# Kernel optimization log

Measured on AMD Instinct MI355X. Metric: run time of the kernel, lower is better.

## Reference

```python
import jax, jax.numpy as jnp
import numpy as np
import math

B, S, D_MODEL = 4, 2048, 1024
H, D_QK, D_V = 16, 64, 64


def setup_inputs() -> dict:
    key = jax.random.key(0)
    ks = jax.random.split(key, 12)
    s = 0.02
    return {
        "input_q": jax.random.normal(ks[0], (B, S, D_MODEL), jnp.float32),
        "input_k": jax.random.normal(ks[1], (B, S, D_MODEL), jnp.float32),
        "input_v": jax.random.normal(ks[2], (B, S, D_MODEL), jnp.float32),
        # per-head projection weights stacked over heads: [H, out, d_model] (torch Linear layout)
        "WQw": jax.random.normal(ks[3], (H, D_QK, D_MODEL), jnp.float32) * s,
        "WQb": jax.random.normal(ks[4], (H, D_QK), jnp.float32) * s,
        "WKw": jax.random.normal(ks[5], (H, D_QK, D_MODEL), jnp.float32) * s,
        "WKb": jax.random.normal(ks[6], (H, D_QK), jnp.float32) * s,
        "WVw": jax.random.normal(ks[7], (H, D_V, D_MODEL), jnp.float32) * s,
        "WVb": jax.random.normal(ks[8], (H, D_V), jnp.float32) * s,
        # output projection: Linear(H*D_V, D_MODEL)
        "Ww": jax.random.normal(ks[9], (D_MODEL, H * D_V), jnp.float32) * s,
        "Wb": jax.random.normal(ks[10], (D_MODEL,), jnp.float32) * s,
    }


def _mha(input_q, input_k, input_v, WQw, WQb, WKw, WKb, WVw, WVb, Ww, Wb):
    # per-head projections: [B,H,S,d]
    Q = jnp.einsum("bsd,hed->bhse", input_q, WQw) + WQb[None, :, None, :]
    K = jnp.einsum("bsd,hed->bhse", input_k, WKw) + WKb[None, :, None, :]
    V = jnp.einsum("bsd,hvd->bhsv", input_v, WVw) + WVb[None, :, None, :]
    scores = jnp.einsum("bhse,bhte->bhst", Q, K)  # [B,H,S,S]
    # causal mask added BEFORE division by sqrt(d_model), as in original
    causal = jnp.triu(jnp.full((S, S), -jnp.inf, scores.dtype), k=1)
    scores = (scores + causal) / math.sqrt(D_MODEL)  # NOTE: d_model, not d_qk
    attn = jax.nn.softmax(scores, axis=-1)
    ctx = jnp.einsum("bhst,bhtv->bhsv", attn, V)  # [B,H,S,D_V]
    concat = ctx.transpose(0, 2, 1, 3).reshape(B, S, H * D_V)  # head-order concat
    return concat @ Ww.T + Wb


def reference(input_q, input_k, input_v, WQw, WQb, WKw, WKb, WVw, WVb, Ww, Wb):
    return _mha(input_q, input_k, input_v, WQw, WQb, WKw, WKb, WVw, WVb, Ww, Wb)
```

## Files before the change

kernel.cpp:

```cpp
#include <hip/hip_runtime.h>
#include <hip/hip_bf16.h>

typedef __attribute__((ext_vector_type(8))) short bf16x8;
typedef __attribute__((ext_vector_type(4))) short bf16x4;
typedef __attribute__((ext_vector_type(4))) float f32x4;
typedef __attribute__((ext_vector_type(16))) float f32x16;

#define MFMA16(a, b, c) __builtin_amdgcn_mfma_f32_16x16x32_bf16(a, b, c, 0, 0, 0)
#define MFMA32(a, b, c) __builtin_amdgcn_mfma_f32_32x32x16_bf16(a, b, c, 0, 0, 0)

__device__ __forceinline__ unsigned short f2bfn(float f) {
#if defined(__gfx950__)
  __bf16 h = (__bf16)f;
  return __builtin_bit_cast(unsigned short, h);
#else
  union { float f; unsigned u; } x; x.f = f;
  unsigned r = x.u + 0x7fffu + ((x.u >> 16) & 1u);
  return (unsigned short)(r >> 16);
#endif
}

__device__ __forceinline__ void plswap(unsigned& a, unsigned& b) {
  auto r = __builtin_amdgcn_permlane32_swap(a, b, false, false);
  a = r[0];
  b = r[1];
}

__device__ __forceinline__ unsigned cvtpk(float lo, float hi) {
  unsigned w;
  asm("v_cvt_pk_bf16_f32 %0, %1, %2" : "=v"(w) : "v"(lo), "v"(hi));
  return w;
}

__device__ __forceinline__ void cvt_body(const float* __restrict__ s,
                                         unsigned short* __restrict__ d, int n8) {
  int i = blockIdx.x * blockDim.x + threadIdx.x;
  int st = gridDim.x * blockDim.x;
  for (; i < n8; i += st) {
    const float4* sp = reinterpret_cast<const float4*>(s) + 2 * (size_t)i;
    float4 a = sp[0], b = sp[1];
    bf16x8 o;
    o[0] = (short)f2bfn(a.x); o[1] = (short)f2bfn(a.y);
    o[2] = (short)f2bfn(a.z); o[3] = (short)f2bfn(a.w);
    o[4] = (short)f2bfn(b.x); o[5] = (short)f2bfn(b.y);
    o[6] = (short)f2bfn(b.z); o[7] = (short)f2bfn(b.w);
    reinterpret_cast<bf16x8*>(d)[i] = o;
  }
}

__global__ void cvt1_kernel(const float* __restrict__ s, unsigned short* __restrict__ d, int n8) {
  cvt_body(s, d, n8);
}

__global__ void cvt_w_kernel(const float* s0, const float* s1, const float* s2, const float* s3,
                             unsigned short* d0, unsigned short* d1, unsigned short* d2,
                             unsigned short* d3, int n8) {
  const float* s; unsigned short* d;
  switch (blockIdx.y) {
    case 0: s = s0; d = d0; break;
    case 1: s = s1; d = d1; break;
    case 2: s = s2; d = d2; break;
    default: s = s3; d = d3; break;
  }
  cvt_body(s, d, n8);
}

template <int MODE>
__global__ __launch_bounds__(256) void gemm_kernel(
    const unsigned short* __restrict__ Av, const unsigned short* __restrict__ Bv,
    const float* __restrict__ bias, void* __restrict__ outv,
    int M, int N, int K) {
  constexpr int BM = 128, BN = 128, BK = 64;
  __shared__ __align__(16) unsigned short As[2][BM * BK];
  __shared__ __align__(16) unsigned short Bs[2][BN * BK];
  const int tid = threadIdx.x;
  const int lane = tid & 63, wave = tid >> 6;
  const int wr = wave >> 1, wc = wave & 1;
  const int m0 = blockIdx.y * BM, n0 = blockIdx.x * BN;
  const int rb = lane & 15, g = lane >> 4;
  const int swz = ((lane & 7) ^ ((lane >> 3) & 7)) * 8;
  f32x4 acc[4][4] = {};

  const unsigned short* Ab = Av + (size_t)m0 * K;
  const unsigned short* Bb = Bv + (size_t)n0 * K;

  auto stage = [&](int buf, int k0) {
#pragma unroll
    for (int i = 0; i < 4; ++i) {
      const int c = wave * 256 + i * 64 + lane;
      const int r = c >> 3;
      __builtin_amdgcn_global_load_lds(
          (const __attribute__((address_space(1))) unsigned int*)(Ab + (size_t)r * K + k0 + swz),
          (__attribute__((address_space(3))) unsigned int*)&As[buf][c * 8], 16, 0, 0);
      __builtin_amdgcn_global_load_lds(
          (const __attribute__((address_space(1))) unsigned int*)(Bb + (size_t)r * K + k0 + swz),
          (__attribute__((address_space(3))) unsigned int*)&Bs[buf][c * 8], 16, 0, 0);
    }
  };

  const int nt = K / BK;
  stage(0, 0);
  int cur = 0;
  for (int t = 0; t < nt; ++t) {
    __syncthreads();
    if (t + 1 < nt) stage(cur ^ 1, (t + 1) * BK);
    const unsigned short* A_ = As[cur];
    const unsigned short* B_ = Bs[cur];
#pragma unroll
    for (int kc = 0; kc < 2; ++kc) {
      bf16x8 af[4], bfr[4];
#pragma unroll
      for (int mi = 0; mi < 4; ++mi)
        af[mi] = *reinterpret_cast<const bf16x8*>(
            &A_[(wr * 64 + mi * 16 + rb) * 64 + (((kc * 4 + g) ^ (rb & 7)) * 8)]);
#pragma unroll
      for (int ni = 0; ni < 4; ++ni)
        bfr[ni] = *reinterpret_cast<const bf16x8*>(
            &B_[(wc * 64 + ni * 16 + rb) * 64 + (((kc * 4 + g) ^ (rb & 7)) * 8)]);
#pragma unroll
      for (int mi = 0; mi < 4; ++mi)
#pragma unroll
        for (int ni = 0; ni < 4; ++ni)
          acc[mi][ni] = MFMA16(af[mi], bfr[ni], acc[mi][ni]);
    }
    cur ^= 1;
  }

#pragma unroll
  for (int mi = 0; mi < 4; ++mi) {
#pragma unroll
    for (int ni = 0; ni < 4; ++ni) {
      int col = n0 + wc * 64 + ni * 16 + rb;
      if constexpr (MODE != 2) {
        float bv = bias[col];
#pragma unroll
        for (int j = 0; j < 4; ++j) {
          int row = m0 + wr * 64 + mi * 16 + g * 4 + j;
          float v = acc[mi][ni][j] + bv;
          if constexpr (MODE == 0) {
            int b = row >> 11, s = row & 2047;
            int h = col >> 6, e = col & 63;
            ((unsigned short*)outv)[((size_t)(b * 16 + h) * 2048 + s) * 64 + e] = f2bfn(v);
          } else {
            ((float*)outv)[(size_t)row * N + col] = v;
          }
        }
      } else {
        int bb = col >> 11, s = col & 2047;
#pragma unroll
        for (int j = 0; j < 4; ++j) {
          int row = m0 + wr * 64 + mi * 16 + g * 4 + j;
          float v = acc[mi][ni][j] + bias[row];
          int h = row >> 6, e = row & 63;
          ((unsigned short*)outv)[((size_t)(bb * 16 + h) * 64 + e) * 2048 + s] = f2bfn(v);
        }
      }
    }
  }
}

__global__ __launch_bounds__(256) void attn3_kernel(
    const unsigned short* __restrict__ Qp, const unsigned short* __restrict__ Kp,
    const unsigned short* __restrict__ Vtp, unsigned short* __restrict__ ctx) {
  constexpr int S = 2048;
  __shared__ __align__(16) unsigned short Ks[2][64 * 64];
  __shared__ __align__(16) unsigned short Vs[2][64 * 64];
  const int bx = blockIdx.x;
  const int bh = bx & 63;
  const int qti = 15 - (bx >> 6);
  const int q0 = qti * 128;
  const int tid = threadIdx.x, wave = tid >> 6, lane = tid & 63;
  const int l31 = lane & 31, hb = lane >> 5, hb4 = hb * 4;
  const int x7 = l31 & 7;
  const int qw = q0 + wave * 32;
  const unsigned short* Qb = Qp + (size_t)bh * S * 64;
  const unsigned short* Kb = Kp + (size_t)bh * S * 64;
  const unsigned short* Vb = Vtp + (size_t)bh * 64 * S;

  bf16x8 qg[4];
#pragma unroll
  for (int kc = 0; kc < 4; ++kc)
    qg[kc] = *reinterpret_cast<const bf16x8*>(
        Qb + (size_t)(qw + l31) * 64 + 16 * kc + 8 * hb);

  float m2 = -1e30f, nm2 = 0.f, lsum = 0.f;
  f32x16 o[2] = {};
  const float sc = 0.03125f * 1.4426950408889634f;
  const float TH = 8.0f / sc;
  const int sswz = ((lane & 7) ^ (lane >> 3)) * 8;
  const int nt = qti * 2 + 2;

  auto stage = [&](int buf, int kv0) {
#pragma unroll
    for (int i = 0; i < 2; ++i) {
      const int ci = (wave * 2 + i) * 64 + lane;
      const int r = (wave * 2 + i) * 8 + (lane >> 3);
      __builtin_amdgcn_global_load_lds(
          (const __attribute__((address_space(1))) unsigned int*)(Kb + (size_t)(kv0 + r) * 64 + sswz),
          (__attribute__((address_space(3))) unsigned int*)&Ks[buf][ci * 8], 16, 0, 0);
      __builtin_amdgcn_global_load_lds(
          (const __attribute__((address_space(1))) unsigned int*)(Vb + (size_t)r * S + kv0 + sswz),
          (__attribute__((address_space(3))) unsigned int*)&Vs[buf][ci * 8], 16, 0, 0);
    }
  };

  stage(0, 0);

  for (int it = 0; it < nt; ++it) {
    __syncthreads();
    if (it + 1 < nt) stage((it + 1) & 1, 64 * (it + 1));
    const int kv0 = 64 * it;
    if (kv0 <= qw + 31) {
      const unsigned short* K_ = Ks[it & 1];
      const unsigned short* V_ = Vs[it & 1];
      f32x16 sacc[2] = {};
      __builtin_amdgcn_s_setprio(1);
#pragma unroll
      for (int kc = 0; kc < 4; ++kc) {
        bf16x8 kf0 = *reinterpret_cast<const bf16x8*>(
            &K_[l31 * 64 + ((2 * kc + hb) ^ x7) * 8]);
        bf16x8 kf1 = *reinterpret_cast<const bf16x8*>(
            &K_[(32 + l31) * 64 + ((2 * kc + hb) ^ x7) * 8]);
        sacc[0] = MFMA32(kf0, qg[kc], sacc[0]);
        sacc[1] = MFMA32(kf1, qg[kc], sacc[1]);
      }
      __builtin_amdgcn_s_setprio(0);
      if (kv0 + 63 > qw) {
        const int qrel = qw + l31 - kv0;
#pragma unroll
        for (int mi = 0; mi < 2; ++mi)
#pragma unroll
          for (int r = 0; r < 16; ++r) {
            int koff = 32 * mi + (r & 3) + 8 * (r >> 2) + hb4;
            if (koff > qrel) sacc[mi][r] = -1e30f;
          }
      }
      float mt = -1e30f;
#pragma unroll
      for (int mi = 0; mi < 2; ++mi)
#pragma unroll
        for (int r = 0; r < 16; ++r) mt = fmaxf(mt, sacc[mi][r]);
      mt = fmaxf(mt, __shfl_xor(mt, 32, 64));
      if (__any((int)(mt > m2 + TH))) {
        float mn = fmaxf(m2, mt);
        float corr = __builtin_amdgcn_exp2f((m2 - mn) * sc);
        m2 = mn; nm2 = -mn * sc;
        lsum *= corr;
#pragma unroll
        for (int db = 0; db < 2; ++db)
#pragma unroll
          for (int r = 0; r < 16; ++r) o[db][r] *= corr;
      }
      float rs = 0.f;
      unsigned pw[2][8];
#pragma unroll
      for (int mi = 0; mi < 2; ++mi) {
        float p[16];
#pragma unroll
        for (int r = 0; r < 16; ++r) {
          p[r] = __builtin_amdgcn_exp2f(fmaf(sacc[mi][r], sc, nm2));
          rs += p[r];
        }
#pragma unroll
        for (int i = 0; i < 8; ++i) pw[mi][i] = cvtpk(p[2 * i], p[2 * i + 1]);
      }
      lsum += rs;
#pragma unroll
      for (int mi = 0; mi < 2; ++mi) {
        plswap(pw[mi][0], pw[mi][2]);
        plswap(pw[mi][1], pw[mi][3]);
        plswap(pw[mi][4], pw[mi][6]);
        plswap(pw[mi][5], pw[mi][7]);
      }
      __builtin_amdgcn_s_setprio(1);
#pragma unroll
      for (int c = 0; c < 4; ++c) {
        union { unsigned u[4]; bf16x8 v; } pu;
        pu.u[0] = pw[c >> 1][(c & 1) * 4 + 0];
        pu.u[1] = pw[c >> 1][(c & 1) * 4 + 1];
        pu.u[2] = pw[c >> 1][(c & 1) * 4 + 2];
        pu.u[3] = pw[c >> 1][(c & 1) * 4 + 3];
#pragma unroll
        for (int db = 0; db < 2; ++db) {
          bf16x8 vf = *reinterpret_cast<const bf16x8*>(
              &V_[(32 * db + l31) * 64 + ((2 * c + hb) ^ x7) * 8]);
          o[db] = MFMA32(vf, pu.v, o[db]);
        }
      }
      __builtin_amdgcn_s_setprio(0);
    }
  }

  const float tot = lsum + __shfl_xor(lsum, 32, 64);
  const float inv = 1.0f / tot;
  const int b = bh >> 4, h = bh & 15;
  const int q = qw + l31;
  unsigned short* cp = ctx + ((size_t)(b * 2048 + q) * 1024) + h * 64;
#pragma unroll
  for (int db = 0; db < 2; ++db)
#pragma unroll
    for (int i = 0; i < 8; ++i) {
      unsigned w = cvtpk(o[db][2 * i] * inv, o[db][2 * i + 1] * inv);
      int d = 32 * db + ((2 * i) & 3) + 8 * (i >> 1) + hb4;
      *reinterpret_cast<unsigned*>(cp + d) = w;
    }
}

extern "C" void kernel_launch(void* const* d_in, const int* in_sizes, int n_in,
                              void* d_out, int out_size, void* d_ws, size_t ws_size,
                              hipStream_t stream) {
  const float* in_q = (const float*)d_in[0];
  const float* in_k = (const float*)d_in[1];
  const float* in_v = (const float*)d_in[2];
  const float* WQw = (const float*)d_in[3];
  const float* WQb = (const float*)d_in[4];
  const float* WKw = (const float*)d_in[5];
  const float* WKb = (const float*)d_in[6];
  const float* WVw = (const float*)d_in[7];
  const float* WVb = (const float*)d_in[8];
  const float* Ww  = (const float*)d_in[9];
  const float* Wb  = (const float*)d_in[10];
  float* out = (float*)d_out;

  constexpr size_t PROJ = (size_t)4 * 16 * 2048 * 64;
  constexpr size_t WSZ = (size_t)1024 * 1024;
  unsigned short* wsp = (unsigned short*)d_ws;
  unsigned short* Qp   = wsp;
  unsigned short* Kp   = wsp + PROJ;
  unsigned short* Vt   = wsp + 2 * PROJ;
  unsigned short* in16 = wsp + 3 * PROJ;
  unsigned short* ctx  = in16;
  unsigned short* wq16 = wsp + 4 * PROJ;
  unsigned short* wk16 = wq16 + WSZ;
  unsigned short* wv16 = wk16 + WSZ;
  unsigned short* ww16 = wv16 + WSZ;

  cvt_w_kernel<<<dim3(256, 4), 256, 0, stream>>>(WQw, WKw, WVw, Ww,
                                                 wq16, wk16, wv16, ww16, (int)(WSZ / 8));
  cvt1_kernel<<<2048, 256, 0, stream>>>(in_q, in16, (int)(PROJ / 8));
  gemm_kernel<0><<<dim3(8, 64), 256, 0, stream>>>(in16, wq16, WQb, Qp, 8192, 1024, 1024);
  cvt1_kernel<<<2048, 256, 0, stream>>>(in_k, in16, (int)(PROJ / 8));
  gemm_kernel<0><<<dim3(8, 64), 256, 0, stream>>>(in16, wk16, WKb, Kp, 8192, 1024, 1024);
  cvt1_kernel<<<2048, 256, 0, stream>>>(in_v, in16, (int)(PROJ / 8));
  gemm_kernel<2><<<dim3(64, 8), 256, 0, stream>>>(wv16, in16, WVb, Vt, 1024, 8192, 1024);

  attn3_kernel<<<1024, 256, 0, stream>>>(Qp, Kp, Vt, ctx);

  gemm_kernel<1><<<dim3(8, 64), 256, 0, stream>>>(ctx, ww16, Wb, out, 8192, 1024, 1024);
}
```

Baseline: 192.5 us.

## Fuse fp32→bf16 input conversion into projection GEMMs and pair causal attention tiles

The projection GEMMs now read fp32 activations directly, converting to bf16 in registers and writing swizzled tiles to LDS. This removes the three separate conversion kernels and their bf16 intermediate round-trip through global memory. The attention kernel now runs half as many blocks, each handling a long and a short causal query tile so per-block work is balanced, and the softmax max and sum use tree reductions. The weight conversion uses packed cvt instructions. In exchange, the fp32 path re-reads the wider fp32 data for every N-tile and relies on synchronous register staging instead of async global-to-LDS loads, which adds register pressure.

```diff
diff --git a/kernel.cpp b/kernel.cpp
--- a/kernel.cpp
+++ b/kernel.cpp
@@ -5,6 +5,7 @@
 typedef __attribute__((ext_vector_type(4))) short bf16x4;
 typedef __attribute__((ext_vector_type(4))) float f32x4;
 typedef __attribute__((ext_vector_type(16))) float f32x16;
+typedef __attribute__((ext_vector_type(4))) unsigned uint4v;
 
 #define MFMA16(a, b, c) __builtin_amdgcn_mfma_f32_16x16x32_bf16(a, b, c, 0, 0, 0)
 #define MFMA32(a, b, c) __builtin_amdgcn_mfma_f32_32x32x16_bf16(a, b, c, 0, 0, 0)
@@ -39,17 +40,11 @@
   for (; i < n8; i += st) {
     const float4* sp = reinterpret_cast<const float4*>(s) + 2 * (size_t)i;
     float4 a = sp[0], b = sp[1];
-    bf16x8 o;
-    o[0] = (short)f2bfn(a.x); o[1] = (short)f2bfn(a.y);
-    o[2] = (short)f2bfn(a.z); o[3] = (short)f2bfn(a.w);
-    o[4] = (short)f2bfn(b.x); o[5] = (short)f2bfn(b.y);
-    o[6] = (short)f2bfn(b.z); o[7] = (short)f2bfn(b.w);
-    reinterpret_cast<bf16x8*>(d)[i] = o;
-  }
-}
-
-__global__ void cvt1_kernel(const float* __restrict__ s, unsigned short* __restrict__ d, int n8) {
-  cvt_body(s, d, n8);
+    uint4v o;
+    o[0] = cvtpk(a.x, a.y); o[1] = cvtpk(a.z, a.w);
+    o[2] = cvtpk(b.x, b.y); o[3] = cvtpk(b.z, b.w);
+    reinterpret_cast<uint4v*>(d)[i] = o;
+  }
 }
 
 __global__ void cvt_w_kernel(const float* s0, const float* s1, const float* s2, const float* s3,
@@ -67,9 +62,11 @@
 
 template <int MODE>
 __global__ __launch_bounds__(256) void gemm_kernel(
-    const unsigned short* __restrict__ Av, const unsigned short* __restrict__ Bv,
+    const void* __restrict__ Av, const void* __restrict__ Bv,
     const float* __restrict__ bias, void* __restrict__ outv,
     int M, int N, int K) {
+  constexpr bool AF32 = (MODE == 0);
+  constexpr bool BF32 = (MODE == 2);
   constexpr int BM = 128, BN = 128, BK = 64;
   __shared__ __align__(16) unsigned short As[2][BM * BK];
   __shared__ __align__(16) unsigned short Bs[2][BN * BK];
@@ -79,31 +76,68 @@
   const int m0 = blockIdx.y * BM, n0 = blockIdx.x * BN;
   const int rb = lane & 15, g = lane >> 4;
   const int swz = ((lane & 7) ^ ((lane >> 3) & 7)) * 8;
+  const int srow = tid >> 1, scol = (tid & 1) * 32;
   f32x4 acc[4][4] = {};
 
-  const unsigned short* Ab = Av + (size_t)m0 * K;
-  const unsigned short* Bb = Bv + (size_t)n0 * K;
-
-  auto stage = [&](int buf, int k0) {
+  const unsigned short* Ab16 = (const unsigned short*)Av + (size_t)m0 * K;
+  const unsigned short* Bb16 = (const unsigned short*)Bv + (size_t)n0 * K;
+  const float* Ab32 = (const float*)Av + (size_t)m0 * K;
+  const float* Bb32 = (const float*)Bv + (size_t)n0 * K;
+
+  auto gload = [&](const unsigned short* base, unsigned short* dst, int k0) {
 #pragma unroll
     for (int i = 0; i < 4; ++i) {
       const int c = wave * 256 + i * 64 + lane;
       const int r = c >> 3;
       __builtin_amdgcn_global_load_lds(
-          (const __attribute__((address_space(1))) unsigned int*)(Ab + (size_t)r * K + k0 + swz),
-          (__attribute__((address_space(3))) unsigned int*)&As[buf][c * 8], 16, 0, 0);
-      __builtin_amdgcn_global_load_lds(
-          (const __attribute__((address_space(1))) unsigned int*)(Bb + (size_t)r * K + k0 + swz),
-          (__attribute__((address_space(3))) unsigned int*)&Bs[buf][c * 8], 16, 0, 0);
+          (const __attribute__((address_space(1))) unsigned int*)(base + (size_t)r * K + k0 + swz),
+          (__attribute__((address_space(3))) unsigned int*)&dst[c * 8], 16, 0, 0);
     }
   };
+  auto f32load = [&](const float* base, int k0, float4* av) {
+#pragma unroll
+    for (int w = 0; w < 8; ++w)
+      av[w] = *reinterpret_cast<const float4*>(base + (size_t)srow * K + k0 + scol + 4 * w);
+  };
+  auto stwr = [&](unsigned short* T, const float4* av) {
+#pragma unroll
+    for (int w = 0; w < 4; ++w) {
+      const float4 x = av[2 * w], y = av[2 * w + 1];
+      uint4v o;
+      o[0] = cvtpk(x.x, x.y); o[1] = cvtpk(x.z, x.w);
+      o[2] = cvtpk(y.x, y.y); o[3] = cvtpk(y.z, y.w);
+      const int ch = (scol >> 3) + w;
+      *reinterpret_cast<uint4v*>(&T[srow * 64 + ((ch ^ (srow & 7)) * 8)]) = o;
+    }
+  };
 
   const int nt = K / BK;
-  stage(0, 0);
+  if constexpr (AF32) {
+    float4 av[8];
+    f32load(Ab32, 0, av);
+    stwr(As[0], av);
+  } else {
+    gload(Ab16, As[0], 0);
+  }
+  if constexpr (BF32) {
+    float4 bv[8];
+    f32load(Bb32, 0, bv);
+    stwr(Bs[0], bv);
+  } else {
+    gload(Bb16, Bs[0], 0);
+  }
+
   int cur = 0;
   for (int t = 0; t < nt; ++t) {
     __syncthreads();
-    if (t + 1 < nt) stage(cur ^ 1, (t + 1) * BK);
+    const bool more = (t + 1 < nt);
+    float4 avn[8], bvn[8];
+    if (more) {
+      if constexpr (AF32) f32load(Ab32, (t + 1) * BK, avn);
+      else gload(Ab16, As[cur ^ 1], (t + 1) * BK);
+      if constexpr (BF32) f32load(Bb32, (t + 1) * BK, bvn);
+      else gload(Bb16, Bs[cur ^ 1], (t + 1) * BK);
+    }
     const unsigned short* A_ = As[cur];
     const unsigned short* B_ = Bs[cur];
 #pragma unroll
@@ -122,6 +156,10 @@
 #pragma unroll
         for (int ni = 0; ni < 4; ++ni)
           acc[mi][ni] = MFMA16(af[mi], bfr[ni], acc[mi][ni]);
+    }
+    if (more) {
+      if constexpr (AF32) stwr(As[cur ^ 1], avn);
+      if constexpr (BF32) stwr(Bs[cur ^ 1], bvn);
     }
     cur ^= 1;
   }
@@ -167,28 +205,16 @@
   __shared__ __align__(16) unsigned short Vs[2][64 * 64];
   const int bx = blockIdx.x;
   const int bh = bx & 63;
-  const int qti = 15 - (bx >> 6);
-  const int q0 = qti * 128;
+  const int pi = bx >> 6;
   const int tid = threadIdx.x, wave = tid >> 6, lane = tid & 63;
   const int l31 = lane & 31, hb = lane >> 5, hb4 = hb * 4;
   const int x7 = l31 & 7;
-  const int qw = q0 + wave * 32;
   const unsigned short* Qb = Qp + (size_t)bh * S * 64;
   const unsigned short* Kb = Kp + (size_t)bh * S * 64;
   const unsigned short* Vb = Vtp + (size_t)bh * 64 * S;
-
-  bf16x8 qg[4];
-#pragma unroll
-  for (int kc = 0; kc < 4; ++kc)
-    qg[kc] = *reinterpret_cast<const bf16x8*>(
-        Qb + (size_t)(qw + l31) * 64 + 16 * kc + 8 * hb);
-
-  float m2 = -1e30f, nm2 = 0.f, lsum = 0.f;
-  f32x16 o[2] = {};
   const float sc = 0.03125f * 1.4426950408889634f;
   const float TH = 8.0f / sc;
   const int sswz = ((lane & 7) ^ (lane >> 3)) * 8;
-  const int nt = qti * 2 + 2;
 
   auto stage = [&](int buf, int kv0) {
 #pragma unroll
@@ -204,106 +230,130 @@
     }
   };
 
-  stage(0, 0);
-
-  for (int it = 0; it < nt; ++it) {
+  for (int half = 0; half < 2; ++half) {
+    const int qti = half ? pi : 15 - pi;
+    const int qw = qti * 128 + wave * 32;
+
+    bf16x8 qg[4];
+#pragma unroll
+    for (int kc = 0; kc < 4; ++kc)
+      qg[kc] = *reinterpret_cast<const bf16x8*>(
+          Qb + (size_t)(qw + l31) * 64 + 16 * kc + 8 * hb);
+
+    float m2 = -1e30f, nm2 = 0.f, lsum = 0.f;
+    f32x16 o[2] = {};
+    const int nt = qti * 2 + 2;
+
     __syncthreads();
-    if (it + 1 < nt) stage((it + 1) & 1, 64 * (it + 1));
-    const int kv0 = 64 * it;
-    if (kv0 <= qw + 31) {
-      const unsigned short* K_ = Ks[it & 1];
-      const unsigned short* V_ = Vs[it & 1];
-      f32x16 sacc[2] = {};
-      __builtin_amdgcn_s_setprio(1);
-#pragma unroll
-      for (int kc = 0; kc < 4; ++kc) {
-        bf16x8 kf0 = *reinterpret_cast<const bf16x8*>(
-            &K_[l31 * 64 + ((2 * kc + hb) ^ x7) * 8]);
-        bf16x8 kf1 = *reinterpret_cast<const bf16x8*>(
-            &K_[(32 + l31) * 64 + ((2 * kc + hb) ^ x7) * 8]);
-        sacc[0] = MFMA32(kf0, qg[kc], sacc[0]);
-        sacc[1] = MFMA32(kf1, qg[kc], sacc[1]);
+    stage(0, 0);
+
+    for (int it = 0; it < nt; ++it) {
+      __syncthreads();
+      if (it + 1 < nt) stage((it + 1) & 1, 64 * (it + 1));
+      const int kv0 = 64 * it;
+      if (kv0 <= qw + 31) {
+        const unsigned short* K_ = Ks[it & 1];
+        const unsigned short* V_ = Vs[it & 1];
+        f32x16 sacc[2] = {};
+        __builtin_amdgcn_s_setprio(1);
+#pragma unroll
+        for (int kc = 0; kc < 4; ++kc) {
+          bf16x8 kf0 = *reinterpret_cast<const bf16x8*>(
+              &K_[l31 * 64 + ((2 * kc + hb) ^ x7) * 8]);
+          bf16x8 kf1 = *reinterpret_cast<const bf16x8*>(
+              &K_[(32 + l31) * 64 + ((2 * kc + hb) ^ x7) * 8]);
+          sacc[0] = MFMA32(kf0, qg[kc], sacc[0]);
+          sacc[1] = MFMA32(kf1, qg[kc], sacc[1]);
+        }
+        __builtin_amdgcn_s_setprio(0);
+        if (kv0 + 63 > qw) {
+          const int qrel = qw + l31 - kv0;
+#pragma unroll
+          for (int mi = 0; mi < 2; ++mi)
+#pragma unroll
+            for (int r = 0; r < 16; ++r) {
+              int koff = 32 * mi + (r & 3) + 8 * (r >> 2) + hb4;
+              if (koff > qrel) sacc[mi][r] = -1e30f;
+            }
+        }
+        float mx[16];
+#pragma unroll
+        for (int r = 0; r < 16; ++r) mx[r] = fmaxf(sacc[0][r], sacc[1][r]);
+#pragma unroll
+        for (int s = 8; s > 0; s >>= 1)
+#pragma unroll
+          for (int r = 0; r < s; ++r) mx[r] = fmaxf(mx[r], mx[r + s]);
+        float mt = fmaxf(mx[0], __shfl_xor(mx[0], 32, 64));
+        if (__any((int)(mt > m2 + TH))) {
+          float mn = fmaxf(m2, mt);
+          float corr = __builtin_amdgcn_exp2f((m2 - mn) * sc);
+          m2 = mn; nm2 = -mn * sc;
+          lsum *= corr;
+#pragma unroll
+          for (int db = 0; db < 2; ++db)
+#pragma unroll
+            for (int r = 0; r < 16; ++r) o[db][r] *= corr;
+        }
+        float p0[16], p1[16];
+#pragma unroll
+        for (int r = 0; r < 16; ++r)
+          p0[r] = __builtin_amdgcn_exp2f(fmaf(sacc[0][r], sc, nm2));
+#pragma unroll
+        for (int r = 0; r < 16; ++r)
+          p1[r] = __builtin_amdgcn_exp2f(fmaf(sacc[1][r], sc, nm2));
+        unsigned pw[2][8];
+#pragma unroll
+        for (int i = 0; i < 8; ++i) pw[0][i] = cvtpk(p0[2 * i], p0[2 * i + 1]);
+#pragma unroll
+        for (int i = 0; i < 8; ++i) pw[1][i] = cvtpk(p1[2 * i], p1[2 * i + 1]);
+        float a[16];
+#pragma unroll
+        for (int r = 0; r < 16; ++r) a[r] = p0[r] + p1[r];
+#pragma unroll
+        for (int s = 8; s > 0; s >>= 1)
+#pragma unroll
+          for (int r = 0; r < s; ++r) a[r] += a[r + s];
+        lsum += a[0];
+#pragma unroll
+        for (int mi = 0; mi < 2; ++mi) {
+          plswap(pw[mi][0], pw[mi][2]);
+          plswap(pw[mi][1], pw[mi][3]);
+          plswap(pw[mi][4], pw[mi][6]);
+          plswap(pw[mi][5], pw[mi][7]);
+        }
+        __builtin_amdgcn_s_setprio(1);
+#pragma unroll
+        for (int c = 0; c < 4; ++c) {
+          union { unsigned u[4]; bf16x8 v; } pu;
+          pu.u[0] = pw[c >> 1][(c & 1) * 4 + 0];
+          pu.u[1] = pw[c >> 1][(c & 1) * 4 + 1];
+          pu.u[2] = pw[c >> 1][(c & 1) * 4 + 2];
+          pu.u[3] = pw[c >> 1][(c & 1) * 4 + 3];
+#pragma unroll
+          for (int db = 0; db < 2; ++db) {
+            bf16x8 vf = *reinterpret_cast<const bf16x8*>(
+                &V_[(32 * db + l31) * 64 + ((2 * c + hb) ^ x7) * 8]);
+            o[db] = MFMA32(vf, pu.v, o[db]);
+          }
+        }
+        __builtin_amdgcn_s_setprio(0);
       }
-      __builtin_amdgcn_s_setprio(0);
-      if (kv0 + 63 > qw) {
-        const int qrel = qw + l31 - kv0;
-#pragma unroll
-        for (int mi = 0; mi < 2; ++mi)
-#pragma unroll
-          for (int r = 0; r < 16; ++r) {
-            int koff = 32 * mi + (r & 3) + 8 * (r >> 2) + hb4;
-            if (koff > qrel) sacc[mi][r] = -1e30f;
-          }
+    }
+
+    const float tot = lsum + __shfl_xor(lsum, 32, 64);
+    const float inv = 1.0f / tot;
+    const int b = bh >> 4, h = bh & 15;
+    const int q = qw + l31;
+    unsigned short* cp = ctx + ((size_t)(b * 2048 + q) * 1024) + h * 64;
+#pragma unroll
+    for (int db = 0; db < 2; ++db)
+#pragma unroll
+      for (int i = 0; i < 8; ++i) {
+        unsigned w = cvtpk(o[db][2 * i] * inv, o[db][2 * i + 1] * inv);
+        int d = 32 * db + ((2 * i) & 3) + 8 * (i >> 1) + hb4;
+        *reinterpret_cast<unsigned*>(cp + d) = w;
       }
-      float mt = -1e30f;
-#pragma unroll
-      for (int mi = 0; mi < 2; ++mi)
-#pragma unroll
-        for (int r = 0; r < 16; ++r) mt = fmaxf(mt, sacc[mi][r]);
-      mt = fmaxf(mt, __shfl_xor(mt, 32, 64));
-      if (__any((int)(mt > m2 + TH))) {
-        float mn = fmaxf(m2, mt);
-        float corr = __builtin_amdgcn_exp2f((m2 - mn) * sc);
-        m2 = mn; nm2 = -mn * sc;
-        lsum *= corr;
-#pragma unroll
-        for (int db = 0; db < 2; ++db)
-#pragma unroll
-          for (int r = 0; r < 16; ++r) o[db][r] *= corr;
-      }
-      float rs = 0.f;
-      unsigned pw[2][8];
-#pragma unroll
-      for (int mi = 0; mi < 2; ++mi) {
-        float p[16];
-#pragma unroll
-        for (int r = 0; r < 16; ++r) {
-          p[r] = __builtin_amdgcn_exp2f(fmaf(sacc[mi][r], sc, nm2));
-          rs += p[r];
-        }
-#pragma unroll
-        for (int i = 0; i < 8; ++i) pw[mi][i] = cvtpk(p[2 * i], p[2 * i + 1]);
-      }
-      lsum += rs;
-#pragma unroll
-      for (int mi = 0; mi < 2; ++mi) {
-        plswap(pw[mi][0], pw[mi][2]);
-        plswap(pw[mi][1], pw[mi][3]);
-        plswap(pw[mi][4], pw[mi][6]);
-        plswap(pw[mi][5], pw[mi][7]);
-      }
-      __builtin_amdgcn_s_setprio(1);
-#pragma unroll
-      for (int c = 0; c < 4; ++c) {
-        union { unsigned u[4]; bf16x8 v; } pu;
-        pu.u[0] = pw[c >> 1][(c & 1) * 4 + 0];
-        pu.u[1] = pw[c >> 1][(c & 1) * 4 + 1];
-        pu.u[2] = pw[c >> 1][(c & 1) * 4 + 2];
-        pu.u[3] = pw[c >> 1][(c & 1) * 4 + 3];
-#pragma unroll
-        for (int db = 0; db < 2; ++db) {
-          bf16x8 vf = *reinterpret_cast<const bf16x8*>(
-              &V_[(32 * db + l31) * 64 + ((2 * c + hb) ^ x7) * 8]);
-          o[db] = MFMA32(vf, pu.v, o[db]);
-        }
-      }
-      __builtin_amdgcn_s_setprio(0);
-    }
-  }
-
-  const float tot = lsum + __shfl_xor(lsum, 32, 64);
-  const float inv = 1.0f / tot;
-  const int b = bh >> 4, h = bh & 15;
-  const int q = qw + l31;
-  unsigned short* cp = ctx + ((size_t)(b * 2048 + q) * 1024) + h * 64;
-#pragma unroll
-  for (int db = 0; db < 2; ++db)
-#pragma unroll
-    for (int i = 0; i < 8; ++i) {
-      unsigned w = cvtpk(o[db][2 * i] * inv, o[db][2 * i + 1] * inv);
-      int d = 32 * db + ((2 * i) & 3) + 8 * (i >> 1) + hb4;
-      *reinterpret_cast<unsigned*>(cp + d) = w;
-    }
+  }
 }
 
 extern "C" void kernel_launch(void* const* d_in, const int* in_sizes, int n_in,
@@ -328,8 +378,7 @@
   unsigned short* Qp   = wsp;
   unsigned short* Kp   = wsp + PROJ;
   unsigned short* Vt   = wsp + 2 * PROJ;
-  unsigned short* in16 = wsp + 3 * PROJ;
-  unsigned short* ctx  = in16;
+  unsigned short* ctx  = wsp + 3 * PROJ;
   unsigned short* wq16 = wsp + 4 * PROJ;
   unsigned short* wk16 = wq16 + WSZ;
   unsigned short* wv16 = wk16 + WSZ;
@@ -337,14 +386,11 @@
 
   cvt_w_kernel<<<dim3(256, 4), 256, 0, stream>>>(WQw, WKw, WVw, Ww,
                                                  wq16, wk16, wv16, ww16, (int)(WSZ / 8));
-  cvt1_kernel<<<2048, 256, 0, stream>>>(in_q, in16, (int)(PROJ / 8));
-  gemm_kernel<0><<<dim3(8, 64), 256, 0, stream>>>(in16, wq16, WQb, Qp, 8192, 1024, 1024);
-  cvt1_kernel<<<2048, 256, 0, stream>>>(in_k, in16, (int)(PROJ / 8));
-  gemm_kernel<0><<<dim3(8, 64), 256, 0, stream>>>(in16, wk16, WKb, Kp, 8192, 1024, 1024);
-  cvt1_kernel<<<2048, 256, 0, stream>>>(in_v, in16, (int)(PROJ / 8));
-  gemm_kernel<2><<<dim3(64, 8), 256, 0, stream>>>(wv16, in16, WVb, Vt, 1024, 8192, 1024);
-
-  attn3_kernel<<<1024, 256, 0, stream>>>(Qp, Kp, Vt, ctx);
+  gemm_kernel<0><<<dim3(8, 64), 256, 0, stream>>>(in_q, wq16, WQb, Qp, 8192, 1024, 1024);
+  gemm_kernel<0><<<dim3(8, 64), 256, 0, stream>>>(in_k, wk16, WKb, Kp, 8192, 1024, 1024);
+  gemm_kernel<2><<<dim3(64, 8), 256, 0, stream>>>(wv16, in_v, WVb, Vt, 1024, 8192, 1024);
+
+  attn3_kernel<<<512, 256, 0, stream>>>(Qp, Kp, Vt, ctx);
 
   gemm_kernel<1><<<dim3(8, 64), 256, 0, stream>>>(ctx, ww16, Wb, out, 8192, 1024, 1024);
 }
```

Measured after the change: 240.8 us. +25.1%, slower.
